# Performance work log

Measured on AMD Instinct MI355X. Metric: run time of the kernel, lower is better.

The kernel has to match this reference:

```python
import jax, jax.numpy as jnp
import numpy as np

CHUNK = 128  # chunk size for the causal linear-attention recurrence
EPS = 1e-10


def _causal_numerator(q, k, v, chunk=CHUNK):
    """N_i = sum_{j<=i} (q_i . k_j) v_j, computed chunk-recurrently.

    q,k: [B,H,N,D]; v: [B,H,N,E] -> [B,H,N,E]
    """
    B, H, N, D = q.shape
    E = v.shape[-1]
    nc = N // chunk
    qc = jnp.moveaxis(q.reshape(B, H, nc, chunk, D), 2, 0)  # [nc,B,H,c,D]
    kc = jnp.moveaxis(k.reshape(B, H, nc, chunk, D), 2, 0)
    vc = jnp.moveaxis(v.reshape(B, H, nc, chunk, E), 2, 0)
    mask = jnp.tril(jnp.ones((chunk, chunk), dtype=q.dtype))  # causal within chunk

    def step(S, inp):  # S: running sum of k_j (outer) v_j -> [B,H,D,E]
        qi, ki, vi = inp
        scores = jnp.einsum('bhid,bhjd->bhij', qi, ki) * mask
        intra = jnp.einsum('bhij,bhje->bhie', scores, vi)
        inter = jnp.einsum('bhid,bhde->bhie', qi, S)
        S = S + jnp.einsum('bhjd,bhje->bhde', ki, vi)
        return S, intra + inter

    S0 = jnp.zeros((B, H, D, E), q.dtype)
    _, outs = jax.lax.scan(step, S0, (qc, kc, vc))  # [nc,B,H,c,E]
    return jnp.moveaxis(outs, 0, 2).reshape(B, H, N, E)


def _causal_denominator(q, k):
    # D_i = q_i . cumsum_j<=i k_j  -> [B,H,N]
    return jnp.einsum('bhnd,bhnd->bhn', q, jnp.cumsum(k, axis=-2))


def setup_inputs() -> dict:
    key = jax.random.key(0)
    ks = jax.random.split(key, 5)
    shape = (2, 8, 4096, 64)
    names = ['q', 'k', 'q_rot', 'k_rot', 'v']
    # feature-mapped inputs (Performer softmax features) are positive
    return {n: jax.random.uniform(ks[i], shape, dtype=jnp.float32) for i, n in enumerate(names)}


def reference(q, k, q_rot, k_rot, v):
    N = _causal_numerator(q, k, v) + _causal_numerator(q_rot, k_rot, v)
    D = _causal_denominator(q, k) + _causal_denominator(q_rot, k_rot)
    return N * (1.0 / (D + EPS))[..., None]
```

## Files before the change

kernel.cpp:

```cpp
#include <hip/hip_runtime.h>

#define SEQ 4096
#define DIM 64
#define CHUNK 128
#define NC 32
#define EPSV 1e-10f
#define KS_OFF 2097152

typedef __attribute__((ext_vector_type(8))) short s16x8;
typedef __attribute__((ext_vector_type(4))) float f32x4;

__device__ __forceinline__ unsigned short f2bf(float f) {
  unsigned int u = __float_as_uint(f);
  u += 0x7FFF + ((u >> 16) & 1);
  return (unsigned short)(u >> 16);
}
__device__ __forceinline__ float bf2f(unsigned short s) {
  return __uint_as_float(((unsigned int)s) << 16);
}
__device__ __forceinline__ s16x8 pack8(float4 a, float4 b) {
  s16x8 r;
  r[0] = (short)f2bf(a.x); r[1] = (short)f2bf(a.y); r[2] = (short)f2bf(a.z); r[3] = (short)f2bf(a.w);
  r[4] = (short)f2bf(b.x); r[5] = (short)f2bf(b.y); r[6] = (short)f2bf(b.z); r[7] = (short)f2bf(b.w);
  return r;
}

__device__ __forceinline__ void stage_nat(const float* __restrict__ gp,
                                          unsigned short* __restrict__ nat, int t) {
#pragma unroll
  for (int p = 0; p < 8; ++p) {
    int idx = t + p * 256;
    int i = idx >> 4, d4 = idx & 15;
    float4 x = ((const float4*)gp)[idx];
    ushort4 u = make_ushort4(f2bf(x.x), f2bf(x.y), f2bf(x.z), f2bf(x.w));
    *(ushort4*)&nat[i * 72 + d4 * 4] = u;
  }
}

__device__ __forceinline__ void transpose_to_T(const unsigned short* __restrict__ nat,
                                               unsigned short* __restrict__ dst, int t) {
  int L = t & 63, w = t >> 6;
#pragma unroll
  for (int it = 0; it < 4; ++it) {
    int d = L, j8 = it * 4 + w;
    s16x8 seg;
#pragma unroll
    for (int u = 0; u < 8; ++u) seg[u] = (short)nat[(j8 * 8 + u) * 72 + d];
    *(s16x8*)&dst[d * 136 + j8 * 8] = seg;
  }
}

__global__ __launch_bounds__(256) void pass_a(const float* __restrict__ k0,
                                              const float* __restrict__ k1,
                                              const float* __restrict__ v,
                                              float* __restrict__ ws) {
  __shared__ __align__(16) unsigned short skT[64 * 136];
  __shared__ __align__(16) unsigned short svT[64 * 136];
  __shared__ __align__(16) unsigned short snat[128 * 72];
  int bid = blockIdx.x;
  int m = bid >> 9, rem = bid & 511, hh = rem >> 5, c = rem & 31;
  const float* kp = (m ? k1 : k0) + (size_t)hh * SEQ * DIM + (size_t)c * CHUNK * DIM;
  const float* vp = v + (size_t)hh * SEQ * DIM + (size_t)c * CHUNK * DIM;
  int t = threadIdx.x;

  stage_nat(kp, snat, t);
  __syncthreads();
  transpose_to_T(snat, skT, t);
  __syncthreads();
  stage_nat(vp, snat, t);
  __syncthreads();
  transpose_to_T(snat, svT, t);
  __syncthreads();

  if (t < 64) {
    float s = 0.f;
    for (int it = 0; it < 16; ++it) {
      s16x8 blk = *(const s16x8*)&skT[t * 136 + it * 8];
#pragma unroll
      for (int u = 0; u < 8; ++u) s += bf2f((unsigned short)blk[u]);
    }
    ws[KS_OFF + (size_t)bid * 64 + t] = s;
  }

  int w = t >> 6, L = t & 63, g = L >> 4, cL = L & 15;
  f32x4 acc[4];
#pragma unroll
  for (int ct = 0; ct < 4; ++ct) acc[ct] = (f32x4){0.f, 0.f, 0.f, 0.f};
#pragma unroll
  for (int ks = 0; ks < 4; ++ks) {
    s16x8 aF = *(const s16x8*)&svT[(w * 16 + cL) * 136 + ks * 32 + g * 8];
#pragma unroll
    for (int ct = 0; ct < 4; ++ct) {
      s16x8 bF = *(const s16x8*)&skT[(ct * 16 + cL) * 136 + ks * 32 + g * 8];
      acc[ct] = __builtin_amdgcn_mfma_f32_16x16x32_bf16(aF, bF, acc[ct], 0, 0, 0);
    }
  }
  unsigned short* Sp = (unsigned short*)ws + (size_t)bid * 4096;
#pragma unroll
  for (int ct = 0; ct < 4; ++ct)
#pragma unroll
    for (int r = 0; r < 4; ++r)
      Sp[(size_t)(w * 16 + g * 4 + r) * 64 + ct * 16 + cL] = f2bf(acc[ct][r]);
}

__global__ __launch_bounds__(256) void pass_b(float* __restrict__ ws) {
  int t = threadIdx.x;
  if (blockIdx.x < 256) {
    int gid = blockIdx.x * 256 + t;
    int mh = gid >> 11, de2 = gid & 2047;
    unsigned int* p = (unsigned int*)ws + (size_t)mh * NC * 2048 + de2;
    unsigned int x[NC];
#pragma unroll
    for (int c = 0; c < NC; ++c) x[c] = p[(size_t)c * 2048];
    float r0 = 0.f, r1 = 0.f;
#pragma unroll
    for (int c = 0; c < NC; ++c) {
      unsigned int xc = x[c];
      p[(size_t)c * 2048] = (unsigned int)f2bf(r0) | ((unsigned int)f2bf(r1) << 16);
      r0 += bf2f((unsigned short)(xc & 0xFFFF));
      r1 += bf2f((unsigned short)(xc >> 16));
    }
  } else {
    int gid = (blockIdx.x - 256) * 256 + t;
    int mh = gid >> 6, d = gid & 63;
    float* p = ws + KS_OFF + (size_t)mh * NC * 64 + d;
    float x[NC];
#pragma unroll
    for (int c = 0; c < NC; ++c) x[c] = p[(size_t)c * 64];
    float run = 0.f;
#pragma unroll
    for (int c = 0; c < NC; ++c) {
      p[(size_t)c * 64] = run;
      run += x[c];
    }
  }
}

__global__ __launch_bounds__(256) void pass_c(const float* __restrict__ q0,
                                              const float* __restrict__ q1,
                                              const float* __restrict__ k0,
                                              const float* __restrict__ k1,
                                              const float* __restrict__ v,
                                              const float* __restrict__ ws,
                                              float* __restrict__ out) {
  __shared__ __align__(16) unsigned short svT[64 * 136];
  __shared__ __align__(16) unsigned short sun[128 * 72];
  __shared__ float skpref[64];
  __shared__ float sden[128];

  int hh = blockIdx.x >> 5, c = blockIdx.x & 31;
  int t = threadIdx.x;
  int w = t >> 6, L = t & 63, g = L >> 4, cL = L & 15;
  size_t off = (size_t)hh * SEQ * DIM + (size_t)c * CHUNK * DIM;
  int rt_of[2] = {w, 7 - w};

  stage_nat(v + off, sun, t);
  __syncthreads();
  transpose_to_T(sun, svT, t);

  f32x4 accO[2][4];
#pragma unroll
  for (int a = 0; a < 2; ++a)
#pragma unroll
    for (int b = 0; b < 4; ++b) accO[a][b] = (f32x4){0.f, 0.f, 0.f, 0.f};
  float denfrag[2][4] = {};
  float denp[2] = {0.f, 0.f};

  const unsigned short* Sbase = (const unsigned short*)ws;

  for (int m = 0; m < 2; ++m) {
    const float* qp = (m ? q1 : q0) + off;
    const float* kp = (m ? k1 : k0) + off;
    const unsigned short* Sp = Sbase + (size_t)(m * 512 + hh * 32 + c) * 4096;
    const float* Kp = ws + KS_OFF + (size_t)(m * 512 + hh * 32 + c) * 64;

    __syncthreads();
#pragma unroll
    for (int p2 = 0; p2 < 2; ++p2) {
      int idx = t + p2 * 256;
      int e = idx >> 3, seg = idx & 7;
      *(s16x8*)&sun[e * 72 + seg * 8] = *(const s16x8*)&Sp[idx * 8];
    }
    if (t < 64) skpref[t] = Kp[t];
    __syncthreads();

    float kpf[2][8];
#pragma unroll
    for (int h = 0; h < 2; ++h) {
      float4 c0 = *(const float4*)&skpref[h * 32 + g * 8];
      float4 c1 = *(const float4*)&skpref[h * 32 + g * 8 + 4];
      kpf[h][0] = c0.x; kpf[h][1] = c0.y; kpf[h][2] = c0.z; kpf[h][3] = c0.w;
      kpf[h][4] = c1.x; kpf[h][5] = c1.y; kpf[h][6] = c1.z; kpf[h][7] = c1.w;
    }

    s16x8 aq[2][2];
#pragma unroll
    for (int ti = 0; ti < 2; ++ti) {
      int row = rt_of[ti] * 16 + cL;
#pragma unroll
      for (int h = 0; h < 2; ++h) {
        const float* qa = qp + row * 64 + h * 32 + g * 8;
        float4 a0 = *(const float4*)qa;
        float4 a1 = *(const float4*)(qa + 4);
        denp[ti] += a0.x * kpf[h][0] + a0.y * kpf[h][1] + a0.z * kpf[h][2] + a0.w * kpf[h][3]
                  + a1.x * kpf[h][4] + a1.y * kpf[h][5] + a1.z * kpf[h][6] + a1.w * kpf[h][7];
        aq[ti][h] = pack8(a0, a1);
      }
    }

#pragma unroll
    for (int h = 0; h < 2; ++h) {
#pragma unroll
      for (int et = 0; et < 4; ++et) {
        s16x8 bS = *(const s16x8*)&sun[(et * 16 + cL) * 72 + h * 32 + g * 8];
        accO[0][et] = __builtin_amdgcn_mfma_f32_16x16x32_bf16(aq[0][h], bS, accO[0][et], 0, 0, 0);
        accO[1][et] = __builtin_amdgcn_mfma_f32_16x16x32_bf16(aq[1][h], bS, accO[1][et], 0, 0, 0);
      }
    }
    __syncthreads();

    for (int s = 0; s <= (7 - w) >> 1; ++s) {
      s16x8 bK[2][2];
#pragma unroll
      for (int ct01 = 0; ct01 < 2; ++ct01) {
        int jrow = (2 * s + ct01) * 16 + cL;
#pragma unroll
        for (int h = 0; h < 2; ++h) {
          const float* ka = kp + jrow * 64 + h * 32 + g * 8;
          float4 b0 = *(const float4*)ka;
          float4 b1 = *(const float4*)(ka + 4);
          bK[ct01][h] = pack8(b0, b1);
        }
      }
#pragma unroll
      for (int ti = 0; ti < 2; ++ti) {
        int rt = rt_of[ti];
        if (2 * s > rt) continue;
        int rowbase = rt * 16 + g * 4;
#pragma unroll
        for (int ct01 = 0; ct01 < 2; ++ct01) {
          int jt = 2 * s + ct01;
          if (jt > rt) {
#pragma unroll
            for (int r = 0; r < 4; ++r) sun[(rowbase + r) * 40 + ct01 * 16 + cL] = 0;
          } else {
            f32x4 C = (f32x4){0.f, 0.f, 0.f, 0.f};
            C = __builtin_amdgcn_mfma_f32_16x16x32_bf16(aq[ti][0], bK[ct01][0], C, 0, 0, 0);
            C = __builtin_amdgcn_mfma_f32_16x16x32_bf16(aq[ti][1], bK[ct01][1], C, 0, 0, 0);
            if (jt == rt) {
#pragma unroll
              for (int r = 0; r < 4; ++r)
                if (cL > g * 4 + r) C[r] = 0.f;
            }
#pragma unroll
            for (int r = 0; r < 4; ++r) {
              denfrag[ti][r] += C[r];
              sun[(rowbase + r) * 40 + ct01 * 16 + cL] = f2bf(C[r]);
            }
          }
        }
      }
      asm volatile("s_waitcnt lgkmcnt(0)" ::: "memory");

      s16x8 bV[4];
#pragma unroll
      for (int et = 0; et < 4; ++et)
        bV[et] = *(const s16x8*)&svT[(et * 16 + cL) * 136 + s * 32 + g * 8];
#pragma unroll
      for (int ti = 0; ti < 2; ++ti) {
        if (2 * s > rt_of[ti]) continue;
        s16x8 aP = *(const s16x8*)&sun[(rt_of[ti] * 16 + cL) * 40 + g * 8];
#pragma unroll
        for (int et = 0; et < 4; ++et)
          accO[ti][et] = __builtin_amdgcn_mfma_f32_16x16x32_bf16(aP, bV[et], accO[ti][et], 0, 0, 0);
      }
    }
  }

#pragma unroll
  for (int ti = 0; ti < 2; ++ti) {
    denp[ti] += __shfl_xor(denp[ti], 16);
    denp[ti] += __shfl_xor(denp[ti], 32);
  }
  if (L < 16) {
    sden[rt_of[0] * 16 + L] = denp[0];
    sden[rt_of[1] * 16 + L] = denp[1];
  }
  __syncthreads();

  float* op = out + off;
#pragma unroll
  for (int ti = 0; ti < 2; ++ti) {
#pragma unroll
    for (int r = 0; r < 4; ++r) {
      float vs = denfrag[ti][r];
      vs += __shfl_xor(vs, 1);
      vs += __shfl_xor(vs, 2);
      vs += __shfl_xor(vs, 4);
      vs += __shfl_xor(vs, 8);
      int row = rt_of[ti] * 16 + g * 4 + r;
      float inv = 1.f / (sden[row] + vs + EPSV);
#pragma unroll
      for (int et = 0; et < 4; ++et)
        op[(size_t)row * 64 + et * 16 + cL] = accO[ti][et][r] * inv;
    }
  }
}

extern "C" void kernel_launch(void* const* d_in, const int* in_sizes, int n_in,
                              void* d_out, int out_size, void* d_ws, size_t ws_size,
                              hipStream_t stream) {
  const float* q  = (const float*)d_in[0];
  const float* k  = (const float*)d_in[1];
  const float* qr = (const float*)d_in[2];
  const float* kr = (const float*)d_in[3];
  const float* v  = (const float*)d_in[4];
  float* out = (float*)d_out;
  float* ws  = (float*)d_ws;

  hipLaunchKernelGGL(pass_a, dim3(1024), dim3(256), 0, stream, k, kr, v, ws);
  hipLaunchKernelGGL(pass_b, dim3(264), dim3(256), 0, stream, ws);
  hipLaunchKernelGGL(pass_c, dim3(512), dim3(256), 0, stream, q, qr, k, kr, v, ws, out);
}
```

Measured before the change: 140.4 us.

## Halve chunk size to 64 and give each warp one 16-row tile

Shrinks the recurrence chunk from 128 to 64 rows. This doubles the number of blocks in the state-building and output passes, and the prefix-scan pass now walks 64 chunk states instead of 32. In the output kernel each wave handles a single 16-row tile instead of a load-balanced pair. LDS footprint is smaller, and launch bounds ask for 4 blocks per CU to raise occupancy. The cost is twice as many per-chunk state matrices to write, scan and read, plus a longer per-thread register array in the scan kernel.

```diff
diff --git a/kernel.cpp b/kernel.cpp
--- a/kernel.cpp
+++ b/kernel.cpp
@@ -2,10 +2,10 @@
 
 #define SEQ 4096
 #define DIM 64
-#define CHUNK 128
-#define NC 32
+#define HC 64
+#define NHC 64
 #define EPSV 1e-10f
-#define KS_OFF 2097152
+#define KS_OFF 4194304
 
 typedef __attribute__((ext_vector_type(8))) short s16x8;
 typedef __attribute__((ext_vector_type(4))) float f32x4;
@@ -25,10 +25,10 @@
   return r;
 }
 
-__device__ __forceinline__ void stage_nat(const float* __restrict__ gp,
-                                          unsigned short* __restrict__ nat, int t) {
-#pragma unroll
-  for (int p = 0; p < 8; ++p) {
+__device__ __forceinline__ void stage_nat64(const float* __restrict__ gp,
+                                            unsigned short* __restrict__ nat, int t) {
+#pragma unroll
+  for (int p = 0; p < 4; ++p) {
     int idx = t + p * 256;
     int i = idx >> 4, d4 = idx & 15;
     float4 x = ((const float4*)gp)[idx];
@@ -37,16 +37,16 @@
   }
 }
 
-__device__ __forceinline__ void transpose_to_T(const unsigned short* __restrict__ nat,
-                                               unsigned short* __restrict__ dst, int t) {
+__device__ __forceinline__ void transpose64(const unsigned short* __restrict__ nat,
+                                            unsigned short* __restrict__ dst, int t) {
   int L = t & 63, w = t >> 6;
 #pragma unroll
-  for (int it = 0; it < 4; ++it) {
+  for (int it = 0; it < 2; ++it) {
     int d = L, j8 = it * 4 + w;
     s16x8 seg;
 #pragma unroll
     for (int u = 0; u < 8; ++u) seg[u] = (short)nat[(j8 * 8 + u) * 72 + d];
-    *(s16x8*)&dst[d * 136 + j8 * 8] = seg;
+    *(s16x8*)&dst[d * 72 + j8 * 8] = seg;
   }
 }
 
@@ -54,28 +54,29 @@
                                               const float* __restrict__ k1,
                                               const float* __restrict__ v,
                                               float* __restrict__ ws) {
-  __shared__ __align__(16) unsigned short skT[64 * 136];
-  __shared__ __align__(16) unsigned short svT[64 * 136];
-  __shared__ __align__(16) unsigned short snat[128 * 72];
+  __shared__ __align__(16) unsigned short skT[64 * 72];
+  __shared__ __align__(16) unsigned short svT[64 * 72];
+  __shared__ __align__(16) unsigned short snat[64 * 72];
   int bid = blockIdx.x;
-  int m = bid >> 9, rem = bid & 511, hh = rem >> 5, c = rem & 31;
-  const float* kp = (m ? k1 : k0) + (size_t)hh * SEQ * DIM + (size_t)c * CHUNK * DIM;
-  const float* vp = v + (size_t)hh * SEQ * DIM + (size_t)c * CHUNK * DIM;
+  int m = bid >> 10, hh = (bid >> 6) & 15, hc = bid & 63;
+  const float* kp = (m ? k1 : k0) + (size_t)hh * SEQ * DIM + (size_t)hc * HC * DIM;
+  const float* vp = v + (size_t)hh * SEQ * DIM + (size_t)hc * HC * DIM;
   int t = threadIdx.x;
 
-  stage_nat(kp, snat, t);
-  __syncthreads();
-  transpose_to_T(snat, skT, t);
-  __syncthreads();
-  stage_nat(vp, snat, t);
-  __syncthreads();
-  transpose_to_T(snat, svT, t);
+  stage_nat64(kp, snat, t);
+  __syncthreads();
+  transpose64(snat, skT, t);
+  __syncthreads();
+  stage_nat64(vp, snat, t);
+  __syncthreads();
+  transpose64(snat, svT, t);
   __syncthreads();
 
   if (t < 64) {
     float s = 0.f;
-    for (int it = 0; it < 16; ++it) {
-      s16x8 blk = *(const s16x8*)&skT[t * 136 + it * 8];
+#pragma unroll
+    for (int it = 0; it < 8; ++it) {
+      s16x8 blk = *(const s16x8*)&skT[t * 72 + it * 8];
 #pragma unroll
       for (int u = 0; u < 8; ++u) s += bf2f((unsigned short)blk[u]);
     }
@@ -87,11 +88,11 @@
 #pragma unroll
   for (int ct = 0; ct < 4; ++ct) acc[ct] = (f32x4){0.f, 0.f, 0.f, 0.f};
 #pragma unroll
-  for (int ks = 0; ks < 4; ++ks) {
-    s16x8 aF = *(const s16x8*)&svT[(w * 16 + cL) * 136 + ks * 32 + g * 8];
+  for (int ks = 0; ks < 2; ++ks) {
+    s16x8 aF = *(const s16x8*)&svT[(w * 16 + cL) * 72 + ks * 32 + g * 8];
 #pragma unroll
     for (int ct = 0; ct < 4; ++ct) {
-      s16x8 bF = *(const s16x8*)&skT[(ct * 16 + cL) * 136 + ks * 32 + g * 8];
+      s16x8 bF = *(const s16x8*)&skT[(ct * 16 + cL) * 72 + ks * 32 + g * 8];
       acc[ct] = __builtin_amdgcn_mfma_f32_16x16x32_bf16(aF, bF, acc[ct], 0, 0, 0);
     }
   }
@@ -108,13 +109,13 @@
   if (blockIdx.x < 256) {
     int gid = blockIdx.x * 256 + t;
     int mh = gid >> 11, de2 = gid & 2047;
-    unsigned int* p = (unsigned int*)ws + (size_t)mh * NC * 2048 + de2;
-    unsigned int x[NC];
-#pragma unroll
-    for (int c = 0; c < NC; ++c) x[c] = p[(size_t)c * 2048];
+    unsigned int* p = (unsigned int*)ws + (size_t)mh * NHC * 2048 + de2;
+    unsigned int x[NHC];
+#pragma unroll
+    for (int c = 0; c < NHC; ++c) x[c] = p[(size_t)c * 2048];
     float r0 = 0.f, r1 = 0.f;
 #pragma unroll
-    for (int c = 0; c < NC; ++c) {
+    for (int c = 0; c < NHC; ++c) {
       unsigned int xc = x[c];
       p[(size_t)c * 2048] = (unsigned int)f2bf(r0) | ((unsigned int)f2bf(r1) << 16);
       r0 += bf2f((unsigned short)(xc & 0xFFFF));
@@ -123,63 +124,61 @@
   } else {
     int gid = (blockIdx.x - 256) * 256 + t;
     int mh = gid >> 6, d = gid & 63;
-    float* p = ws + KS_OFF + (size_t)mh * NC * 64 + d;
-    float x[NC];
-#pragma unroll
-    for (int c = 0; c < NC; ++c) x[c] = p[(size_t)c * 64];
+    float* p = ws + KS_OFF + (size_t)mh * NHC * 64 + d;
+    float x[NHC];
+#pragma unroll
+    for (int c = 0; c < NHC; ++c) x[c] = p[(size_t)c * 64];
     float run = 0.f;
 #pragma unroll
-    for (int c = 0; c < NC; ++c) {
+    for (int c = 0; c < NHC; ++c) {
       p[(size_t)c * 64] = run;
       run += x[c];
     }
   }
 }
 
-__global__ __launch_bounds__(256) void pass_c(const float* __restrict__ q0,
-                                              const float* __restrict__ q1,
-                                              const float* __restrict__ k0,
-                                              const float* __restrict__ k1,
-                                              const float* __restrict__ v,
-                                              const float* __restrict__ ws,
-                                              float* __restrict__ out) {
-  __shared__ __align__(16) unsigned short svT[64 * 136];
-  __shared__ __align__(16) unsigned short sun[128 * 72];
+__global__ __launch_bounds__(256, 4) void pass_c(const float* __restrict__ q0,
+                                                 const float* __restrict__ q1,
+                                                 const float* __restrict__ k0,
+                                                 const float* __restrict__ k1,
+                                                 const float* __restrict__ v,
+                                                 const float* __restrict__ ws,
+                                                 float* __restrict__ out) {
+  __shared__ __align__(16) unsigned short svT[64 * 72];
+  __shared__ __align__(16) unsigned short sun[64 * 72];
   __shared__ float skpref[64];
-  __shared__ float sden[128];
-
-  int hh = blockIdx.x >> 5, c = blockIdx.x & 31;
+  __shared__ float sden[64];
+
+  int hh = blockIdx.x >> 6, hc = blockIdx.x & 63;
   int t = threadIdx.x;
   int w = t >> 6, L = t & 63, g = L >> 4, cL = L & 15;
-  size_t off = (size_t)hh * SEQ * DIM + (size_t)c * CHUNK * DIM;
-  int rt_of[2] = {w, 7 - w};
-
-  stage_nat(v + off, sun, t);
-  __syncthreads();
-  transpose_to_T(sun, svT, t);
-
-  f32x4 accO[2][4];
-#pragma unroll
-  for (int a = 0; a < 2; ++a)
-#pragma unroll
-    for (int b = 0; b < 4; ++b) accO[a][b] = (f32x4){0.f, 0.f, 0.f, 0.f};
-  float denfrag[2][4] = {};
-  float denp[2] = {0.f, 0.f};
+  size_t off = (size_t)hh * SEQ * DIM + (size_t)hc * HC * DIM;
+
+  stage_nat64(v + off, sun, t);
+  __syncthreads();
+  transpose64(sun, svT, t);
+
+  f32x4 accO[4];
+#pragma unroll
+  for (int b = 0; b < 4; ++b) accO[b] = (f32x4){0.f, 0.f, 0.f, 0.f};
+  float denfrag[4] = {};
+  float denp = 0.f;
 
   const unsigned short* Sbase = (const unsigned short*)ws;
 
   for (int m = 0; m < 2; ++m) {
     const float* qp = (m ? q1 : q0) + off;
     const float* kp = (m ? k1 : k0) + off;
-    const unsigned short* Sp = Sbase + (size_t)(m * 512 + hh * 32 + c) * 4096;
-    const float* Kp = ws + KS_OFF + (size_t)(m * 512 + hh * 32 + c) * 64;
+    int sid = m * 1024 + hh * 64 + hc;
+    const unsigned short* Sp = Sbase + (size_t)sid * 4096;
+    const float* Kp = ws + KS_OFF + (size_t)sid * 64;
 
     __syncthreads();
 #pragma unroll
     for (int p2 = 0; p2 < 2; ++p2) {
       int idx = t + p2 * 256;
       int e = idx >> 3, seg = idx & 7;
-      *(s16x8*)&sun[e * 72 + seg * 8] = *(const s16x8*)&Sp[idx * 8];
+      *(s16x8*)&sun[e * 72 + seg * 8] = ((const s16x8*)Sp)[idx];
     }
     if (t < 64) skpref[t] = Kp[t];
     __syncthreads();
@@ -193,18 +192,17 @@
       kpf[h][4] = c1.x; kpf[h][5] = c1.y; kpf[h][6] = c1.z; kpf[h][7] = c1.w;
     }
 
-    s16x8 aq[2][2];
-#pragma unroll
-    for (int ti = 0; ti < 2; ++ti) {
-      int row = rt_of[ti] * 16 + cL;
+    s16x8 aq[2];
+    {
+      int rl = w * 16 + cL;
 #pragma unroll
       for (int h = 0; h < 2; ++h) {
-        const float* qa = qp + row * 64 + h * 32 + g * 8;
+        const float* qa = qp + rl * 64 + h * 32 + g * 8;
         float4 a0 = *(const float4*)qa;
         float4 a1 = *(const float4*)(qa + 4);
-        denp[ti] += a0.x * kpf[h][0] + a0.y * kpf[h][1] + a0.z * kpf[h][2] + a0.w * kpf[h][3]
-                  + a1.x * kpf[h][4] + a1.y * kpf[h][5] + a1.z * kpf[h][6] + a1.w * kpf[h][7];
-        aq[ti][h] = pack8(a0, a1);
+        denp += a0.x * kpf[h][0] + a0.y * kpf[h][1] + a0.z * kpf[h][2] + a0.w * kpf[h][3]
+              + a1.x * kpf[h][4] + a1.y * kpf[h][5] + a1.z * kpf[h][6] + a1.w * kpf[h][7];
+        aq[h] = pack8(a0, a1);
       }
     }
 
@@ -213,13 +211,12 @@
 #pragma unroll
       for (int et = 0; et < 4; ++et) {
         s16x8 bS = *(const s16x8*)&sun[(et * 16 + cL) * 72 + h * 32 + g * 8];
-        accO[0][et] = __builtin_amdgcn_mfma_f32_16x16x32_bf16(aq[0][h], bS, accO[0][et], 0, 0, 0);
-        accO[1][et] = __builtin_amdgcn_mfma_f32_16x16x32_bf16(aq[1][h], bS, accO[1][et], 0, 0, 0);
+        accO[et] = __builtin_amdgcn_mfma_f32_16x16x32_bf16(aq[h], bS, accO[et], 0, 0, 0);
       }
     }
     __syncthreads();
 
-    for (int s = 0; s <= (7 - w) >> 1; ++s) {
+    for (int s = 0; s <= (w >> 1); ++s) {
       s16x8 bK[2][2];
 #pragma unroll
       for (int ct01 = 0; ct01 < 2; ++ct01) {
@@ -232,78 +229,58 @@
           bK[ct01][h] = pack8(b0, b1);
         }
       }
-#pragma unroll
-      for (int ti = 0; ti < 2; ++ti) {
-        int rt = rt_of[ti];
-        if (2 * s > rt) continue;
-        int rowbase = rt * 16 + g * 4;
-#pragma unroll
-        for (int ct01 = 0; ct01 < 2; ++ct01) {
-          int jt = 2 * s + ct01;
-          if (jt > rt) {
-#pragma unroll
-            for (int r = 0; r < 4; ++r) sun[(rowbase + r) * 40 + ct01 * 16 + cL] = 0;
-          } else {
-            f32x4 C = (f32x4){0.f, 0.f, 0.f, 0.f};
-            C = __builtin_amdgcn_mfma_f32_16x16x32_bf16(aq[ti][0], bK[ct01][0], C, 0, 0, 0);
-            C = __builtin_amdgcn_mfma_f32_16x16x32_bf16(aq[ti][1], bK[ct01][1], C, 0, 0, 0);
-            if (jt == rt) {
-#pragma unroll
-              for (int r = 0; r < 4; ++r)
-                if (cL > g * 4 + r) C[r] = 0.f;
-            }
-#pragma unroll
-            for (int r = 0; r < 4; ++r) {
-              denfrag[ti][r] += C[r];
-              sun[(rowbase + r) * 40 + ct01 * 16 + cL] = f2bf(C[r]);
-            }
+      int rowbase = w * 16 + g * 4;
+#pragma unroll
+      for (int ct01 = 0; ct01 < 2; ++ct01) {
+        int jt = 2 * s + ct01;
+        if (jt > w) {
+#pragma unroll
+          for (int r = 0; r < 4; ++r) sun[(rowbase + r) * 40 + ct01 * 16 + cL] = 0;
+        } else {
+          f32x4 C = (f32x4){0.f, 0.f, 0.f, 0.f};
+          C = __builtin_amdgcn_mfma_f32_16x16x32_bf16(aq[0], bK[ct01][0], C, 0, 0, 0);
+          C = __builtin_amdgcn_mfma_f32_16x16x32_bf16(aq[1], bK[ct01][1], C, 0, 0, 0);
+          if (jt == w) {
+#pragma unroll
+            for (int r = 0; r < 4; ++r)
+              if (cL > g * 4 + r) C[r] = 0.f;
+          }
+#pragma unroll
+          for (int r = 0; r < 4; ++r) {
+            denfrag[r] += C[r];
+            sun[(rowbase + r) * 40 + ct01 * 16 + cL] = f2bf(C[r]);
           }
         }
       }
       asm volatile("s_waitcnt lgkmcnt(0)" ::: "memory");
 
-      s16x8 bV[4];
-#pragma unroll
-      for (int et = 0; et < 4; ++et)
-        bV[et] = *(const s16x8*)&svT[(et * 16 + cL) * 136 + s * 32 + g * 8];
-#pragma unroll
-      for (int ti = 0; ti < 2; ++ti) {
-        if (2 * s > rt_of[ti]) continue;
-        s16x8 aP = *(const s16x8*)&sun[(rt_of[ti] * 16 + cL) * 40 + g * 8];
-#pragma unroll
-        for (int et = 0; et < 4; ++et)
-          accO[ti][et] = __builtin_amdgcn_mfma_f32_16x16x32_bf16(aP, bV[et], accO[ti][et], 0, 0, 0);
-      }
-    }
-  }
-
-#pragma unroll
-  for (int ti = 0; ti < 2; ++ti) {
-    denp[ti] += __shfl_xor(denp[ti], 16);
-    denp[ti] += __shfl_xor(denp[ti], 32);
-  }
-  if (L < 16) {
-    sden[rt_of[0] * 16 + L] = denp[0];
-    sden[rt_of[1] * 16 + L] = denp[1];
-  }
+      s16x8 aP = *(const s16x8*)&sun[(w * 16 + cL) * 40 + g * 8];
+#pragma unroll
+      for (int et = 0; et < 4; ++et) {
+        s16x8 bV = *(const s16x8*)&svT[(et * 16 + cL) * 72 + s * 32 + g * 8];
+        accO[et] = __builtin_amdgcn_mfma_f32_16x16x32_bf16(aP, bV, accO[et], 0, 0, 0);
+      }
+    }
+  }
+
+  denp += __shfl_xor(denp, 16);
+  denp += __shfl_xor(denp, 32);
+  if (L < 16) sden[w * 16 + L] = denp;
   __syncthreads();
 
   float* op = out + off;
 #pragma unroll
-  for (int ti = 0; ti < 2; ++ti) {
-#pragma unroll
-    for (int r = 0; r < 4; ++r) {
-      float vs = denfrag[ti][r];
-      vs += __shfl_xor(vs, 1);
-      vs += __shfl_xor(vs, 2);
-      vs += __shfl_xor(vs, 4);
-      vs += __shfl_xor(vs, 8);
-      int row = rt_of[ti] * 16 + g * 4 + r;
-      float inv = 1.f / (sden[row] + vs + EPSV);
-#pragma unroll
-      for (int et = 0; et < 4; ++et)
-        op[(size_t)row * 64 + et * 16 + cL] = accO[ti][et][r] * inv;
-    }
+  for (int r = 0; r < 4; ++r) {
+    float vs = denfrag[r];
+    vs += __shfl_xor(vs, 1);
+    vs += __shfl_xor(vs, 2);
+    vs += __shfl_xor(vs, 4);
+    vs += __shfl_xor(vs, 8);
+    int rl = w * 16 + g * 4 + r;
+    float inv = 1.f / (sden[rl] + vs + EPSV);
+#pragma unroll
+    for (int et = 0; et < 4; ++et)
+      op[(size_t)rl * 64 + et * 16 + cL] = accO[et][r] * inv;
   }
 }
 
@@ -318,7 +295,7 @@
   float* out = (float*)d_out;
   float* ws  = (float*)d_ws;
 
-  hipLaunchKernelGGL(pass_a, dim3(1024), dim3(256), 0, stream, k, kr, v, ws);
+  hipLaunchKernelGGL(pass_a, dim3(2048), dim3(256), 0, stream, k, kr, v, ws);
   hipLaunchKernelGGL(pass_b, dim3(264), dim3(256), 0, stream, ws);
-  hipLaunchKernelGGL(pass_c, dim3(512), dim3(256), 0, stream, q, qr, k, kr, v, ws, out);
-}
+  hipLaunchKernelGGL(pass_c, dim3(1024), dim3(256), 0, stream, q, qr, k, kr, v, ws, out);
+}
```

After: 143.7 us. 2.4% more time.
